# Performance work log

Hardware: AMD Instinct MI355X
Metric: run time of the kernel (lower is better)

## Reference

```python
import jax, jax.numpy as jnp
import numpy as np

B, T, NTR, NTE = 16, 256, 1024, 256
K0, L0 = 1, 1   # torus T1 ensemble
K1, L1 = 16, 2  # euclidean R2 ensemble


def angle2vector(a):
    return jnp.stack([jnp.sin(a), jnp.cos(a)], axis=-1)


def get_grid(latent_dim, num_basis):
    n = int(round(num_basis ** (1.0 / latent_dim)))
    pts = np.linspace(-np.pi, np.pi, n, endpoint=False)
    grid = np.stack(np.meshgrid(*([pts] * latent_dim), indexing='ij'), axis=-1)
    return jnp.asarray(grid.reshape(1, num_basis, latent_dim), jnp.float32)


def gauss_response(z, rf, coeff, mean, log_var, manifold):
    # z: (B,T,L)  rf: (N,L)  coeff: (1,K)  mean: (1,K,L)  log_var: (1,K,L)
    if manifold == 'torus':
        z = angle2vector(z)        # (B,T,L,2)
        rf = angle2vector(rf)      # (N,L,2)
        mean = angle2vector(mean)  # (1,K,L,2)
        sum_axes = (4, 5)
    else:
        sum_axes = (4,)
    mean = mean - rf[:, None]                  # (N,K,L[,2])
    dist = z[:, :, None, None] - mean[None, None]   # (B,T,N,K,L[,2])
    dist = dist / jnp.exp(log_var)[None, None]
    dist = jnp.sum(dist ** 2, axis=sum_axes)        # (B,T,N,K)
    resp = jnp.sum(jnp.exp(-dist) * coeff[None, None], axis=3)  # (B,T,N)
    return jnp.exp(resp)  # nonlinearity='exp'


def setup_inputs() -> dict:
    key = jax.random.key(0)
    ks = jax.random.split(key, 12)
    two_pi = 2.0 * np.pi
    z0 = jax.random.uniform(ks[0], (B, T, L0), jnp.float32) * two_pi - np.pi
    z1 = jax.random.normal(ks[1], (B, T, L1), jnp.float32)
    # FeatureBasis params (shared=True -> leading dim 1)
    coeff0 = jax.random.normal(ks[2], (1, K0), jnp.float32) * 0.01
    coeff0 = coeff0.at[:, 0].add(1.0)
    mean0 = get_grid(L0, K0)
    log_var0 = jnp.log(jnp.ones((1, K0, L0), jnp.float32) * 10.0)
    coeff1 = jax.random.normal(ks[3], (1, K1), jnp.float32) * 0.01
    coeff1 = coeff1.at[:, 0].add(1.0)
    mean1 = get_grid(L1, K1)
    log_var1 = jnp.log(jnp.ones((1, K1, L1), jnp.float32) * 10.0)
    # receptive fields: torus -> uniform angles, euclidean -> randn
    rf_tr0 = jax.random.uniform(ks[4], (NTR, L0), jnp.float32) * two_pi - np.pi
    rf_te0 = jax.random.uniform(ks[5], (NTE, L0), jnp.float32) * two_pi - np.pi
    rf_tr1 = jax.random.normal(ks[6], (NTR, L1), jnp.float32)
    rf_te1 = jax.random.normal(ks[7], (NTE, L1), jnp.float32)
    ew_tr = jax.random.normal(ks[8], (NTR, 2), jnp.float32)
    ew_te = jax.random.normal(ks[9], (NTE, 2), jnp.float32)
    lfs_tr = jnp.zeros((NTR,), jnp.float32)
    lfs_te = jnp.zeros((NTE,), jnp.float32)
    return dict(z0=z0, z1=z1, coeff0=coeff0, mean0=mean0, log_var0=log_var0,
                coeff1=coeff1, mean1=mean1, log_var1=log_var1,
                rf_tr0=rf_tr0, rf_tr1=rf_tr1, rf_te0=rf_te0, rf_te1=rf_te1,
                ew_tr=ew_tr, ew_te=ew_te, lfs_tr=lfs_tr, lfs_te=lfs_te)


def reference(z0, z1, coeff0, mean0, log_var0, coeff1, mean1, log_var1,
              rf_tr0, rf_tr1, rf_te0, rf_te1, ew_tr, ew_te, lfs_tr, lfs_te):
    sg = jax.lax.stop_gradient
    r_tr = jnp.stack([
        gauss_response(z0, rf_tr0, coeff0, mean0, log_var0, 'torus'),
        gauss_response(z1, rf_tr1, coeff1, mean1, log_var1, 'euclidean'),
    ], axis=3)  # (B,T,NTR,2)
    # shared=True -> test responses use train basis with detached z and basis params
    r_te = jnp.stack([
        gauss_response(sg(z0), rf_te0, sg(coeff0), sg(mean0), sg(log_var0), 'torus'),
        gauss_response(sg(z1), rf_te1, sg(coeff1), sg(mean1), sg(log_var1), 'euclidean'),
    ], axis=3)  # (B,T,NTE,2)
    w_tr = jax.nn.softmax(ew_tr, axis=1)[None, None]
    w_te = jax.nn.softmax(ew_te, axis=1)[None, None]
    out_tr = jnp.sum(w_tr * r_tr, axis=3) * jnp.exp(lfs_tr)[None, None]
    out_te = jnp.sum(w_te * r_te, axis=3) * jnp.exp(lfs_te)[None, None]
    return out_tr.transpose(0, 2, 1), out_te.transpose(0, 2, 1)  # (B,N,T)
```

## Files before the change

kernel.cpp:

```cpp
#include <hip/hip_runtime.h>
#include <math.h>

#define B_ 16
#define T_ 256
#define NTR_ 1024
#define NTE_ 256
#define K1_ 16
#define LOG2E_ 1.44269504088896340736f
#define INV2PI_ 0.15915494309189533577f

typedef __attribute__((ext_vector_type(2))) float v2f;

__global__ __launch_bounds__(256, 5) void decoder_kernel(
    const float* __restrict__ z0,
    const float* __restrict__ z1,
    const float* __restrict__ coeff0,
    const float* __restrict__ mean0,
    const float* __restrict__ log_var0,
    const float* __restrict__ coeff1,
    const float* __restrict__ mean1,
    const float* __restrict__ log_var1,
    const float* __restrict__ rf_tr0,
    const float* __restrict__ rf_tr1,
    const float* __restrict__ rf_te0,
    const float* __restrict__ rf_te1,
    const float* __restrict__ ew_tr,
    const float* __restrict__ ew_te,
    const float* __restrict__ lfs_tr,
    const float* __restrict__ lfs_te,
    float* __restrict__ out)
{
    const int bid = blockIdx.x;
    const int t = threadIdx.x;

    const float *rf0, *rf1, *ew, *lfs;
    float* obase;
    int N, n;
    if (bid < NTR_) {
        rf0 = rf_tr0; rf1 = rf_tr1; ew = ew_tr; lfs = lfs_tr;
        obase = out;
        N = NTR_; n = bid;
    } else {
        rf0 = rf_te0; rf1 = rf_te1; ew = ew_te; lfs = lfs_te;
        obase = out + (size_t)B_ * NTR_ * T_;
        N = NTE_; n = bid - NTR_;
    }

    __shared__ float4 s_q0[K1_];
    __shared__ float2 s_q1[K1_];
    __shared__ float s_sc[8];
    if (t < K1_) {
        float rfx = rf1[n * 2 + 0];
        float rfy = rf1[n * 2 + 1];
        float mux = mean1[t * 2 + 0] - rfx;
        float muy = mean1[t * 2 + 1] - rfy;
        float ivx = __expf(-log_var1[t * 2 + 0]);
        float ivy = __expf(-log_var1[t * 2 + 1]);
        float gx = ivx * ivx * LOG2E_;
        float gy = ivy * ivy * LOG2E_;
        s_q0[t] = make_float4(-gx, 2.0f * gx * mux, -gy, 2.0f * gy * muy);
        s_q1[t] = make_float2(-gx * mux * mux - gy * muy * muy,
                              coeff1[t] * LOG2E_);
    }
    if (t == 0) {
        float srf = __builtin_amdgcn_sinf(rf0[n] * INV2PI_);
        float crf = __builtin_amdgcn_cosf(rf0[n] * INV2PI_);
        float sm  = __builtin_amdgcn_sinf(mean0[0] * INV2PI_);
        float cm  = __builtin_amdgcn_cosf(mean0[0] * INV2PI_);
        float s0 = sm - srf;
        float s1 = cm - crf;
        float iv = __expf(-log_var0[0]);
        float q = iv * iv * LOG2E_;
        float nrm2 = s0 * s0 + s1 * s1;
        float Cn = -q * (1.0f + nrm2);
        float Dn = 2.0f * q;
        s_sc[0] = sqrtf(nrm2) * Dn;
        s_sc[1] = -atan2f(s0, s1) * INV2PI_;
        s_sc[2] = Cn;
        s_sc[3] = coeff0[0] * LOG2E_;
        float e0 = ew[n * 2 + 0], e1 = ew[n * 2 + 1];
        float mx = fmaxf(e0, e1);
        float x0 = __expf(e0 - mx), x1 = __expf(e1 - mx);
        float elfs = __expf(lfs[n]) / (x0 + x1);
        s_sc[4] = x0 * elfs;
        s_sc[5] = x1 * elfs;
    }
    __syncthreads();

    v2f X[B_ / 2], Y[B_ / 2], R[B_ / 2];
    const float2* z1v = (const float2*)z1;
#pragma unroll
    for (int j = 0; j < B_ / 2; ++j) {
        float2 p0 = z1v[(2 * j + 0) * T_ + t];
        float2 p1 = z1v[(2 * j + 1) * T_ + t];
        X[j] = (v2f){p0.x, p1.x};
        Y[j] = (v2f){p0.y, p1.y};
        R[j] = (v2f){0.0f, 0.0f};
    }

#pragma unroll
    for (int k = 0; k < K1_; ++k) {
        float4 q0 = s_q0[k];
        float2 q1 = s_q1[k];
        v2f AX = {q0.x, q0.x};
        v2f BX = {q0.y, q0.y};
        v2f AY = {q0.z, q0.z};
        v2f BY = {q0.w, q0.w};
        v2f Cc = {q1.x, q1.x};
        v2f CK = {q1.y, q1.y};
#pragma unroll
        for (int j = 0; j < B_ / 2; ++j) {
            v2f e = __builtin_elementwise_fma(
                X[j], __builtin_elementwise_fma(X[j], AX, BX),
                __builtin_elementwise_fma(Y[j], __builtin_elementwise_fma(Y[j], AY, BY), Cc));
            v2f ex = {__builtin_amdgcn_exp2f(e.x), __builtin_amdgcn_exp2f(e.y)};
            R[j] = __builtin_elementwise_fma(ex, CK, R[j]);
        }
    }

    const float AD = s_sc[0], MPHI = s_sc[1], Cn = s_sc[2], E = s_sc[3];
    const v2f ADv = {AD, AD};
    const v2f CNv = {Cn, Cn};
    const v2f W0 = {s_sc[4], s_sc[4]};
    const v2f W1 = {s_sc[5], s_sc[5]};

#pragma unroll
    for (int j = 0; j < B_ / 2; ++j) {
        float a0 = __fmaf_rn(z0[(2 * j + 0) * T_ + t], INV2PI_, MPHI);
        float a1 = __fmaf_rn(z0[(2 * j + 1) * T_ + t], INV2PI_, MPHI);
        v2f CO = {__builtin_amdgcn_cosf(a0), __builtin_amdgcn_cosf(a1)};
        v2f G = __builtin_elementwise_fma(CO, ADv, CNv);
        v2f R0 = {__builtin_amdgcn_exp2f(__builtin_amdgcn_exp2f(G.x) * E),
                  __builtin_amdgcn_exp2f(__builtin_amdgcn_exp2f(G.y) * E)};
        v2f R1 = {__builtin_amdgcn_exp2f(R[j].x), __builtin_amdgcn_exp2f(R[j].y)};
        v2f O = __builtin_elementwise_fma(W0, R0, W1 * R1);
        obase[(size_t)((2 * j + 0) * N + n) * T_ + t] = O.x;
        obase[(size_t)((2 * j + 1) * N + n) * T_ + t] = O.y;
    }
}

extern "C" void kernel_launch(void* const* d_in, const int* in_sizes, int n_in,
                              void* d_out, int out_size, void* d_ws, size_t ws_size,
                              hipStream_t stream) {
    const float* z0       = (const float*)d_in[0];
    const float* z1       = (const float*)d_in[1];
    const float* coeff0   = (const float*)d_in[2];
    const float* mean0    = (const float*)d_in[3];
    const float* log_var0 = (const float*)d_in[4];
    const float* coeff1   = (const float*)d_in[5];
    const float* mean1    = (const float*)d_in[6];
    const float* log_var1 = (const float*)d_in[7];
    const float* rf_tr0   = (const float*)d_in[8];
    const float* rf_tr1   = (const float*)d_in[9];
    const float* rf_te0   = (const float*)d_in[10];
    const float* rf_te1   = (const float*)d_in[11];
    const float* ew_tr    = (const float*)d_in[12];
    const float* ew_te    = (const float*)d_in[13];
    const float* lfs_tr   = (const float*)d_in[14];
    const float* lfs_te   = (const float*)d_in[15];
    float* out = (float*)d_out;

    int grid = NTR_ + NTE_;
    decoder_kernel<<<grid, T_, 0, stream>>>(
        z0, z1, coeff0, mean0, log_var0, coeff1, mean1, log_var1,
        rf_tr0, rf_tr1, rf_te0, rf_te1, ew_tr, ew_te, lfs_tr, lfs_te, out);
}
```

Before: 103.5 us.

## Factor separable grid Gaussians into recurrence products and vectorize z/out accesses

Exploits the 4x4 uniform grid structure of the euclidean basis means. Each Gaussian factors into x and y terms, which are built by a multiplicative recurrence. This cuts exp2 calls per element from 16 to about 8. The thread mapping changes so each thread handles four consecutive t values for one batch group, using float4 loads and stores. It hardcodes grid layout assumptions (mean1 indexing, K=16) and may reduce precision through chained products.

```diff
diff --git a/kernel.cpp b/kernel.cpp
--- a/kernel.cpp
+++ b/kernel.cpp
@@ -5,11 +5,15 @@
 #define T_ 256
 #define NTR_ 1024
 #define NTE_ 256
-#define K1_ 16
 #define LOG2E_ 1.44269504088896340736f
 #define INV2PI_ 0.15915494309189533577f
 
 typedef __attribute__((ext_vector_type(2))) float v2f;
+
+__device__ __forceinline__ v2f exp2v(v2f a) {
+    return (v2f){__builtin_amdgcn_exp2f(a.x), __builtin_amdgcn_exp2f(a.y)};
+}
+__device__ __forceinline__ v2f splat(float s) { return (v2f){s, s}; }
 
 __global__ __launch_bounds__(256, 5) void decoder_kernel(
     const float* __restrict__ z0,
@@ -31,7 +35,9 @@
     float* __restrict__ out)
 {
     const int bid = blockIdx.x;
-    const int t = threadIdx.x;
+    const int tid = threadIdx.x;
+    const int tq = tid & 63;
+    const int r = tid >> 6;
 
     const float *rf0, *rf1, *ew, *lfs;
     float* obase;
@@ -46,23 +52,36 @@
         N = NTE_; n = bid - NTR_;
     }
 
-    __shared__ float4 s_q0[K1_];
-    __shared__ float2 s_q1[K1_];
-    __shared__ float s_sc[8];
-    if (t < K1_) {
-        float rfx = rf1[n * 2 + 0];
-        float rfy = rf1[n * 2 + 1];
-        float mux = mean1[t * 2 + 0] - rfx;
-        float muy = mean1[t * 2 + 1] - rfy;
-        float ivx = __expf(-log_var1[t * 2 + 0]);
-        float ivy = __expf(-log_var1[t * 2 + 1]);
-        float gx = ivx * ivx * LOG2E_;
-        float gy = ivy * ivy * LOG2E_;
-        s_q0[t] = make_float4(-gx, 2.0f * gx * mux, -gy, 2.0f * gy * muy);
-        s_q1[t] = make_float2(-gx * mux * mux - gy * muy * muy,
-                              coeff1[t] * LOG2E_);
-    }
-    if (t == 0) {
+    __shared__ float4 s_cw[4];
+    __shared__ float s_sc[20];
+    if (tid < 4) {
+        s_cw[tid] = make_float4(coeff1[tid * 4 + 0] * LOG2E_,
+                                coeff1[tid * 4 + 1] * LOG2E_,
+                                coeff1[tid * 4 + 2] * LOG2E_,
+                                coeff1[tid * 4 + 3] * LOG2E_);
+    }
+    if (tid == 0) {
+        float gx = __expf(-2.0f * log_var1[0]) * LOG2E_;
+        float gy = __expf(-2.0f * log_var1[1]) * LOG2E_;
+        float ax = -gx, ay = -gy;
+        float px0 = mean1[0];
+        float hx  = mean1[8] - px0;
+        float py0 = mean1[1];
+        float hy  = mean1[3] - py0;
+        s_sc[6] = ax;
+        s_sc[7] = ay;
+        s_sc[8] = rf1[n * 2 + 0];
+        s_sc[9] = rf1[n * 2 + 1];
+        s_sc[10] = px0;
+        s_sc[11] = py0;
+        s_sc[12] = -2.0f * ax * hx;
+        s_sc[13] = -2.0f * ay * hy;
+        for (int i = 0; i < 3; ++i) {
+            float pxi = px0 + i * hx;
+            float pyi = py0 + i * hy;
+            s_sc[14 + i] = __builtin_amdgcn_exp2f(ax * (2.0f * hx * pxi + hx * hx));
+            s_sc[17 + i] = __builtin_amdgcn_exp2f(ay * (2.0f * hy * pyi + hy * hy));
+        }
         float srf = __builtin_amdgcn_sinf(rf0[n] * INV2PI_);
         float crf = __builtin_amdgcn_cosf(rf0[n] * INV2PI_);
         float sm  = __builtin_amdgcn_sinf(mean0[0] * INV2PI_);
@@ -72,11 +91,9 @@
         float iv = __expf(-log_var0[0]);
         float q = iv * iv * LOG2E_;
         float nrm2 = s0 * s0 + s1 * s1;
-        float Cn = -q * (1.0f + nrm2);
-        float Dn = 2.0f * q;
-        s_sc[0] = sqrtf(nrm2) * Dn;
+        s_sc[0] = sqrtf(nrm2) * 2.0f * q;
         s_sc[1] = -atan2f(s0, s1) * INV2PI_;
-        s_sc[2] = Cn;
+        s_sc[2] = -q * (1.0f + nrm2);
         s_sc[3] = coeff0[0] * LOG2E_;
         float e0 = ew[n * 2 + 0], e1 = ew[n * 2 + 1];
         float mx = fmaxf(e0, e1);
@@ -87,55 +104,85 @@
     }
     __syncthreads();
 
-    v2f X[B_ / 2], Y[B_ / 2], R[B_ / 2];
-    const float2* z1v = (const float2*)z1;
+    const float AD = s_sc[0], MPHI = s_sc[1];
+    const v2f ADv = splat(AD), CNv = splat(s_sc[2]), Ev = splat(s_sc[3]);
+    const v2f W0 = splat(s_sc[4]), W1 = splat(s_sc[5]);
+    const v2f AXv = splat(s_sc[6]), AYv = splat(s_sc[7]);
+    const float rfx = s_sc[8], rfy = s_sc[9];
+    const v2f PX0 = splat(s_sc[10]), PY0 = splat(s_sc[11]);
+    const v2f GXH = splat(s_sc[12]), GYH = splat(s_sc[13]);
+    const v2f KX0 = splat(s_sc[14]), KX1 = splat(s_sc[15]), KX2 = splat(s_sc[16]);
+    const v2f KY0 = splat(s_sc[17]), KY1 = splat(s_sc[18]), KY2 = splat(s_sc[19]);
+
+    const float4* z1q = (const float4*)z1;
+    const float4* z0q = (const float4*)z0;
+    float4* ob4 = (float4*)obase;
+
 #pragma unroll
-    for (int j = 0; j < B_ / 2; ++j) {
-        float2 p0 = z1v[(2 * j + 0) * T_ + t];
-        float2 p1 = z1v[(2 * j + 1) * T_ + t];
-        X[j] = (v2f){p0.x, p1.x};
-        Y[j] = (v2f){p0.y, p1.y};
-        R[j] = (v2f){0.0f, 0.0f};
-    }
-
+    for (int g = 0; g < 4; ++g) {
+        const int b = 4 * g + r;
+        float4 p01 = z1q[b * 128 + 2 * tq];
+        float4 p23 = z1q[b * 128 + 2 * tq + 1];
+        float4 a4  = z0q[b * 64 + tq];
+
+        v2f UXa = {p01.x + rfx, p01.z + rfx};
+        v2f UYa = {p01.y + rfy, p01.w + rfy};
+        v2f UXb = {p23.x + rfx, p23.z + rfx};
+        v2f UYb = {p23.y + rfy, p23.w + rfy};
+
+        v2f dxa = UXa - PX0, dxb = UXb - PX0;
+        v2f dya = UYa - PY0, dyb = UYb - PY0;
+        v2f ExA[4], ExB[4], EyA[4], EyB[4];
+        ExA[0] = exp2v((dxa * AXv) * dxa);
+        ExB[0] = exp2v((dxb * AXv) * dxb);
+        EyA[0] = exp2v((dya * AYv) * dya);
+        EyB[0] = exp2v((dyb * AYv) * dyb);
+        v2f GxA = exp2v(UXa * GXH), GxB = exp2v(UXb * GXH);
+        v2f GyA = exp2v(UYa * GYH), GyB = exp2v(UYb * GYH);
+        ExA[1] = ExA[0] * (GxA * KX0);
+        ExA[2] = ExA[1] * (GxA * KX1);
+        ExA[3] = ExA[2] * (GxA * KX2);
+        ExB[1] = ExB[0] * (GxB * KX0);
+        ExB[2] = ExB[1] * (GxB * KX1);
+        ExB[3] = ExB[2] * (GxB * KX2);
+        EyA[1] = EyA[0] * (GyA * KY0);
+        EyA[2] = EyA[1] * (GyA * KY1);
+        EyA[3] = EyA[2] * (GyA * KY2);
+        EyB[1] = EyB[0] * (GyB * KY0);
+        EyB[2] = EyB[1] * (GyB * KY1);
+        EyB[3] = EyB[2] * (GyB * KY2);
+
+        v2f respA = {0.0f, 0.0f}, respB = {0.0f, 0.0f};
 #pragma unroll
-    for (int k = 0; k < K1_; ++k) {
-        float4 q0 = s_q0[k];
-        float2 q1 = s_q1[k];
-        v2f AX = {q0.x, q0.x};
-        v2f BX = {q0.y, q0.y};
-        v2f AY = {q0.z, q0.z};
-        v2f BY = {q0.w, q0.w};
-        v2f Cc = {q1.x, q1.x};
-        v2f CK = {q1.y, q1.y};
-#pragma unroll
-        for (int j = 0; j < B_ / 2; ++j) {
-            v2f e = __builtin_elementwise_fma(
-                X[j], __builtin_elementwise_fma(X[j], AX, BX),
-                __builtin_elementwise_fma(Y[j], __builtin_elementwise_fma(Y[j], AY, BY), Cc));
-            v2f ex = {__builtin_amdgcn_exp2f(e.x), __builtin_amdgcn_exp2f(e.y)};
-            R[j] = __builtin_elementwise_fma(ex, CK, R[j]);
+        for (int i = 0; i < 4; ++i) {
+            float4 cw = s_cw[i];
+            v2f SA = splat(cw.x) * EyA[0];
+            SA = __builtin_elementwise_fma(splat(cw.y), EyA[1], SA);
+            SA = __builtin_elementwise_fma(splat(cw.z), EyA[2], SA);
+            SA = __builtin_elementwise_fma(splat(cw.w), EyA[3], SA);
+            respA = __builtin_elementwise_fma(ExA[i], SA, respA);
+            v2f SB = splat(cw.x) * EyB[0];
+            SB = __builtin_elementwise_fma(splat(cw.y), EyB[1], SB);
+            SB = __builtin_elementwise_fma(splat(cw.z), EyB[2], SB);
+            SB = __builtin_elementwise_fma(splat(cw.w), EyB[3], SB);
+            respB = __builtin_elementwise_fma(ExB[i], SB, respB);
         }
-    }
-
-    const float AD = s_sc[0], MPHI = s_sc[1], Cn = s_sc[2], E = s_sc[3];
-    const v2f ADv = {AD, AD};
-    const v2f CNv = {Cn, Cn};
-    const v2f W0 = {s_sc[4], s_sc[4]};
-    const v2f W1 = {s_sc[5], s_sc[5]};
-
-#pragma unroll
-    for (int j = 0; j < B_ / 2; ++j) {
-        float a0 = __fmaf_rn(z0[(2 * j + 0) * T_ + t], INV2PI_, MPHI);
-        float a1 = __fmaf_rn(z0[(2 * j + 1) * T_ + t], INV2PI_, MPHI);
-        v2f CO = {__builtin_amdgcn_cosf(a0), __builtin_amdgcn_cosf(a1)};
-        v2f G = __builtin_elementwise_fma(CO, ADv, CNv);
-        v2f R0 = {__builtin_amdgcn_exp2f(__builtin_amdgcn_exp2f(G.x) * E),
-                  __builtin_amdgcn_exp2f(__builtin_amdgcn_exp2f(G.y) * E)};
-        v2f R1 = {__builtin_amdgcn_exp2f(R[j].x), __builtin_amdgcn_exp2f(R[j].y)};
-        v2f O = __builtin_elementwise_fma(W0, R0, W1 * R1);
-        obase[(size_t)((2 * j + 0) * N + n) * T_ + t] = O.x;
-        obase[(size_t)((2 * j + 1) * N + n) * T_ + t] = O.y;
+        v2f R1a = exp2v(respA), R1b = exp2v(respB);
+
+        float aa0 = __fmaf_rn(a4.x, INV2PI_, MPHI);
+        float aa1 = __fmaf_rn(a4.y, INV2PI_, MPHI);
+        float ab0 = __fmaf_rn(a4.z, INV2PI_, MPHI);
+        float ab1 = __fmaf_rn(a4.w, INV2PI_, MPHI);
+        v2f COa = {__builtin_amdgcn_cosf(aa0), __builtin_amdgcn_cosf(aa1)};
+        v2f COb = {__builtin_amdgcn_cosf(ab0), __builtin_amdgcn_cosf(ab1)};
+        v2f Ga = __builtin_elementwise_fma(COa, ADv, CNv);
+        v2f Gb = __builtin_elementwise_fma(COb, ADv, CNv);
+        v2f R0a = exp2v(exp2v(Ga) * Ev);
+        v2f R0b = exp2v(exp2v(Gb) * Ev);
+
+        v2f Oa = __builtin_elementwise_fma(W0, R0a, W1 * R1a);
+        v2f Ob = __builtin_elementwise_fma(W0, R0b, W1 * R1b);
+        ob4[(size_t)(b * N + n) * 64 + tq] = make_float4(Oa.x, Oa.y, Ob.x, Ob.y);
     }
 }
 
```

Measured after the change: 103.2 us. About the same (-0.3%).
